# Performance work log

Hardware: AMD Instinct MI355X
Metric: run time of the kernel (lower is better)

The kernel has to match this reference:

```python
import jax, jax.numpy as jnp
import numpy as np
import math

SQRT2 = math.sqrt(2.0)
SQRT_2PI = math.sqrt(2.0 * math.pi)
T = 1.0


def _margin_from_bn(xt_flat):
    # xt_flat: [B, C*L]. torch .std() is unbiased (ddof=1).
    std = jnp.abs(jnp.std(xt_flat, axis=1, ddof=1))  # [B]
    mean = jnp.mean(xt_flat, axis=1)                  # [B]
    z = -mean / std
    cdf = 0.5 * (1.0 + jax.lax.erf(z / SQRT2))        # norm.cdf(-mean/std)
    safe_cdf = jnp.maximum(cdf, 1e-30)                # guard div; branch selected by where
    margin_a = -std * jnp.exp(-(mean / std) ** 2 / 2.0) / SQRT_2PI / safe_cdf + mean
    margin = jnp.where(cdf > 0.001, margin_a, -3.0 * std)
    # original detaches margin (computed on CPU via numpy/scipy)
    return jax.lax.stop_gradient(margin)


def reference(x_s, x_t, x_ts, x_st, i):
    B, C = x_ts.shape[0], x_ts.shape[1]
    xs = x_ts.reshape(B, C, -1)  # source: [B, C, L]
    xt = x_st.reshape(B, C, -1)  # target: [B, C, L]
    margin = _margin_from_bn(xt.reshape(B, -1))  # [B]
    # distillation_loss(source=xs, target=xt, T, dims=1, margin)
    target = jnp.maximum(xt / T, margin[:, None, None])
    entropy = jax.nn.softmax(xs / T, axis=1) * jax.nn.log_softmax(target / T, axis=1)
    channel_entropy = -jnp.sum(entropy, axis=1)          # [B, L]
    batch_mean_entropy = jnp.mean(channel_entropy, axis=1)  # [B]
    loss = jnp.mean(batch_mean_entropy)
    return (loss, entropy)


def setup_inputs() -> dict:
    key = jax.random.key(0)
    k1, k2, k3, k4 = jax.random.split(key, 4)
    return {
        "x_s": jax.random.normal(k1, (1,), dtype=jnp.float32),
        "x_t": jax.random.normal(k2, (1,), dtype=jnp.float32),
        "x_ts": jax.random.normal(k3, (8, 1024, 64, 64), dtype=jnp.float32),
        "x_st": jax.random.normal(k4, (8, 1024, 64, 64), dtype=jnp.float32),
        "i": 0,
    }
```

## Files before the change

kernel.cpp:

```cpp
#include <hip/hip_runtime.h>
#include <math.h>

#define BB 8
#define CC 1024
#define LL 4096
#define NPB (CC*LL)
#define LT 32


__global__ void k_batch_sums(const float* __restrict__ xt, double* __restrict__ sums) {
    int b = blockIdx.y;
    const float4* p = (const float4*)(xt + (size_t)b * NPB);
    int t = blockIdx.x * blockDim.x + threadIdx.x;
    double s1 = 0.0, s2 = 0.0;
    #pragma unroll
    for (int j4 = 0; j4 < 4; ++j4) {
        float4 v[4];
        #pragma unroll
        for (int k = 0; k < 4; ++k) v[k] = p[(size_t)(j4 * 4 + k) * 65536 + t];
        #pragma unroll
        for (int k = 0; k < 4; ++k) {
            float q1 = (v[k].x + v[k].y) + (v[k].z + v[k].w);
            float q2 = (v[k].x * v[k].x + v[k].y * v[k].y)
                     + (v[k].z * v[k].z + v[k].w * v[k].w);
            s1 += (double)q1;
            s2 += (double)q2;
        }
    }
    for (int off = 32; off; off >>= 1) {
        s1 += __shfl_down(s1, off, 64);
        s2 += __shfl_down(s2, off, 64);
    }
    __shared__ double ls1[4], ls2[4];
    int lane = threadIdx.x & 63, w = threadIdx.x >> 6;
    if (lane == 0) { ls1[w] = s1; ls2[w] = s2; }
    __syncthreads();
    if (threadIdx.x == 0) {
        atomicAdd(&sums[2 * b],     ls1[0] + ls1[1] + ls1[2] + ls1[3]);
        atomicAdd(&sums[2 * b + 1], ls2[0] + ls2[1] + ls2[2] + ls2[3]);
    }
}

__global__ __launch_bounds__(1024)
void k_fused(const float* __restrict__ xs, const float* __restrict__ xt,
             const double* __restrict__ sums,
             float* __restrict__ out1, double* __restrict__ lossAcc) {
    int tid = threadIdx.x;
    int b = blockIdx.y;
    int L0 = blockIdx.x * LT;
    int q = tid & 7;
    int g = tid >> 3;
    int lane = tid & 63, w = tid >> 6;

    __shared__ float s_mg;
    __shared__ __align__(16) float s_red[2][16][8][4];
    __shared__ __align__(16) float s_sinv[8][4];
    __shared__ __align__(16) float s_blog[8][4];
    __shared__ float wacc[16];

    if (tid == 0) {
        double n = (double)NPB;
        double s1 = sums[2 * b], s2 = sums[2 * b + 1];
        double mean = s1 / n;
        double var = (s2 - s1 * s1 / n) / (n - 1.0);
        double sd = sqrt(var);
        double z = -mean / sd;
        double cdf = 0.5 * (1.0 + erf(z / 1.4142135623730951));
        double safe = fmax(cdf, 1e-30);
        double r = mean / sd;
        double ma = -sd * exp(-r * r * 0.5) / 2.5066282746310002 / safe + mean;
        s_mg = (float)((cdf > 0.001) ? ma : -3.0 * sd);
    }
    __syncthreads();
    float mg = s_mg;

    const float* ps = xs + (size_t)b * NPB + L0 + q * 4;
    const float* pt = xt + (size_t)b * NPB + L0 + q * 4;

    float4 es[8], yv[8];
    float ss[4] = {0, 0, 0, 0}, sy[4] = {0, 0, 0, 0};
    #pragma unroll
    for (int i = 0; i < 8; ++i) {
        size_t off = (size_t)(g + 128 * i) * LL;
        float4 s4 = *(const float4*)(ps + off);
        float4 t4 = *(const float4*)(pt + off);
        float4 e, y;
        e.x = __expf(s4.x); e.y = __expf(s4.y); e.z = __expf(s4.z); e.w = __expf(s4.w);
        y.x = fmaxf(t4.x, mg); y.y = fmaxf(t4.y, mg);
        y.z = fmaxf(t4.z, mg); y.w = fmaxf(t4.w, mg);
        es[i] = e; yv[i] = y;
        ss[0] += e.x; ss[1] += e.y; ss[2] += e.z; ss[3] += e.w;
        sy[0] += __expf(y.x); sy[1] += __expf(y.y);
        sy[2] += __expf(y.z); sy[3] += __expf(y.w);
    }
    #pragma unroll
    for (int off = 8; off < 64; off <<= 1) {
        #pragma unroll
        for (int k = 0; k < 4; ++k) {
            ss[k] += __shfl_xor(ss[k], off, 64);
            sy[k] += __shfl_xor(sy[k], off, 64);
        }
    }
    if (lane < 8) {
        #pragma unroll
        for (int k = 0; k < 4; ++k) {
            s_red[0][w][lane][k] = ss[k];
            s_red[1][w][lane][k] = sy[k];
        }
    }
    __syncthreads();
    if (tid < 64) {
        int a  = tid >> 5;
        int qq = (tid >> 2) & 7;
        int k  = tid & 3;
        float t = 0.f;
        #pragma unroll
        for (int ww = 0; ww < 16; ++ww) t += s_red[a][ww][qq][k];
        if (a == 0) s_sinv[qq][k] = 1.0f / t;
        else        s_blog[qq][k] = __logf(t);
    }
    __syncthreads();
    float4 sinv = *(const float4*)&s_sinv[q][0];
    float4 blog = *(const float4*)&s_blog[q][0];

    float* po = out1 + (size_t)b * NPB + L0 + q * 4;
    float acc = 0.f;
    #pragma unroll
    for (int i = 0; i < 8; ++i) {
        size_t off = (size_t)(g + 128 * i) * LL;
        float4 e;
        e.x = es[i].x * sinv.x * (yv[i].x - blog.x);
        e.y = es[i].y * sinv.y * (yv[i].y - blog.y);
        e.z = es[i].z * sinv.z * (yv[i].z - blog.z);
        e.w = es[i].w * sinv.w * (yv[i].w - blog.w);
        *(float4*)(po + off) = e;
        acc += (e.x + e.y) + (e.z + e.w);
    }
    for (int off = 32; off; off >>= 1) acc += __shfl_down(acc, off, 64);
    if (lane == 0) wacc[w] = acc;
    __syncthreads();
    if (tid == 0) {
        double t = 0.0;
        #pragma unroll
        for (int ww = 0; ww < 16; ++ww) t += (double)wacc[ww];
        atomicAdd(lossAcc, t);
    }
}

__global__ void k_finalize(const double* __restrict__ lossAcc, float* __restrict__ out) {
    if (threadIdx.x == 0) out[0] = (float)(-lossAcc[0] / (double)(BB * LL));
}

extern "C" void kernel_launch(void* const* d_in, const int* in_sizes, int n_in,
                              void* d_out, int out_size, void* d_ws, size_t ws_size,
                              hipStream_t stream) {
    const float* x_ts = (const float*)d_in[2];
    const float* x_st = (const float*)d_in[3];
    float* out = (float*)d_out;

    double* sums    = (double*)d_ws;
    double* lossAcc = (double*)((char*)d_ws + 128);

    hipMemsetAsync(d_ws, 0, 256, stream);

    k_batch_sums<<<dim3(256, BB), 256, 0, stream>>>(x_st, sums);
    k_fused<<<dim3(LL / LT, BB), 1024, 0, stream>>>(x_ts, x_st, sums, out + 1, lossAcc);
    k_finalize<<<1, 64, 0, stream>>>(lossAcc, out);
}
```

Before: 391.6 us.

## Stage exp values in LDS, re-read target, halve tile and block size

The fused kernel now handles 16 columns per block with 512 threads, storing exp(source) in a 64KB shared buffer instead of registers. In the second pass it re-reads the target from global memory in reverse channel order, hoping for cache hits, and writes the output with nontemporal stores. The aim is to cut register pressure and raise occupancy. In exchange it adds global read traffic, and the large LDS footprint may limit how many blocks fit per CU.

```diff
diff --git a/kernel.cpp b/kernel.cpp
--- a/kernel.cpp
+++ b/kernel.cpp
@@ -5,7 +5,9 @@
 #define CC 1024
 #define LL 4096
 #define NPB (CC*LL)
-#define LT 32
+#define LT 16
+
+typedef float f32x4 __attribute__((ext_vector_type(4)));
 
 
 __global__ void k_batch_sums(const float* __restrict__ xt, double* __restrict__ sums) {
@@ -41,22 +43,23 @@
     }
 }
 
-__global__ __launch_bounds__(1024)
+__global__ __launch_bounds__(512, 4)
 void k_fused(const float* __restrict__ xs, const float* __restrict__ xt,
              const double* __restrict__ sums,
              float* __restrict__ out1, double* __restrict__ lossAcc) {
     int tid = threadIdx.x;
     int b = blockIdx.y;
     int L0 = blockIdx.x * LT;
-    int q = tid & 7;
-    int g = tid >> 3;
+    int q = tid & 3;
+    int g = tid >> 2;
     int lane = tid & 63, w = tid >> 6;
 
     __shared__ float s_mg;
-    __shared__ __align__(16) float s_red[2][16][8][4];
-    __shared__ __align__(16) float s_sinv[8][4];
-    __shared__ __align__(16) float s_blog[8][4];
-    __shared__ float wacc[16];
+    __shared__ __align__(16) float s_es[CC * LT];
+    __shared__ __align__(16) float s_red[2][8][4][4];
+    __shared__ __align__(16) float s_sinv[4][4];
+    __shared__ __align__(16) float s_blog[4][4];
+    __shared__ float wacc[8];
 
     if (tid == 0) {
         double n = (double)NPB;
@@ -77,31 +80,29 @@
     const float* ps = xs + (size_t)b * NPB + L0 + q * 4;
     const float* pt = xt + (size_t)b * NPB + L0 + q * 4;
 
-    float4 es[8], yv[8];
     float ss[4] = {0, 0, 0, 0}, sy[4] = {0, 0, 0, 0};
     #pragma unroll
     for (int i = 0; i < 8; ++i) {
-        size_t off = (size_t)(g + 128 * i) * LL;
+        int c = g + 128 * i;
+        size_t off = (size_t)c * LL;
         float4 s4 = *(const float4*)(ps + off);
         float4 t4 = *(const float4*)(pt + off);
-        float4 e, y;
+        float4 e;
         e.x = __expf(s4.x); e.y = __expf(s4.y); e.z = __expf(s4.z); e.w = __expf(s4.w);
-        y.x = fmaxf(t4.x, mg); y.y = fmaxf(t4.y, mg);
-        y.z = fmaxf(t4.z, mg); y.w = fmaxf(t4.w, mg);
-        es[i] = e; yv[i] = y;
+        *(float4*)&s_es[c * LT + q * 4] = e;
         ss[0] += e.x; ss[1] += e.y; ss[2] += e.z; ss[3] += e.w;
-        sy[0] += __expf(y.x); sy[1] += __expf(y.y);
-        sy[2] += __expf(y.z); sy[3] += __expf(y.w);
+        sy[0] += __expf(fmaxf(t4.x, mg)); sy[1] += __expf(fmaxf(t4.y, mg));
+        sy[2] += __expf(fmaxf(t4.z, mg)); sy[3] += __expf(fmaxf(t4.w, mg));
     }
     #pragma unroll
-    for (int off = 8; off < 64; off <<= 1) {
+    for (int off = 4; off < 64; off <<= 1) {
         #pragma unroll
         for (int k = 0; k < 4; ++k) {
             ss[k] += __shfl_xor(ss[k], off, 64);
             sy[k] += __shfl_xor(sy[k], off, 64);
         }
     }
-    if (lane < 8) {
+    if (lane < 4) {
         #pragma unroll
         for (int k = 0; k < 4; ++k) {
             s_red[0][w][lane][k] = ss[k];
@@ -109,13 +110,13 @@
         }
     }
     __syncthreads();
-    if (tid < 64) {
-        int a  = tid >> 5;
-        int qq = (tid >> 2) & 7;
+    if (tid < 32) {
+        int a  = tid >> 4;
+        int qq = (tid >> 2) & 3;
         int k  = tid & 3;
         float t = 0.f;
         #pragma unroll
-        for (int ww = 0; ww < 16; ++ww) t += s_red[a][ww][qq][k];
+        for (int ww = 0; ww < 8; ++ww) t += s_red[a][ww][qq][k];
         if (a == 0) s_sinv[qq][k] = 1.0f / t;
         else        s_blog[qq][k] = __logf(t);
     }
@@ -126,14 +127,17 @@
     float* po = out1 + (size_t)b * NPB + L0 + q * 4;
     float acc = 0.f;
     #pragma unroll
-    for (int i = 0; i < 8; ++i) {
-        size_t off = (size_t)(g + 128 * i) * LL;
-        float4 e;
-        e.x = es[i].x * sinv.x * (yv[i].x - blog.x);
-        e.y = es[i].y * sinv.y * (yv[i].y - blog.y);
-        e.z = es[i].z * sinv.z * (yv[i].z - blog.z);
-        e.w = es[i].w * sinv.w * (yv[i].w - blog.w);
-        *(float4*)(po + off) = e;
+    for (int i = 7; i >= 0; --i) {
+        int c = g + 128 * i;
+        size_t off = (size_t)c * LL;
+        float4 t4 = *(const float4*)(pt + off);
+        float4 ev = *(const float4*)&s_es[c * LT + q * 4];
+        f32x4 e;
+        e.x = ev.x * sinv.x * (fmaxf(t4.x, mg) - blog.x);
+        e.y = ev.y * sinv.y * (fmaxf(t4.y, mg) - blog.y);
+        e.z = ev.z * sinv.z * (fmaxf(t4.z, mg) - blog.z);
+        e.w = ev.w * sinv.w * (fmaxf(t4.w, mg) - blog.w);
+        __builtin_nontemporal_store(e, (f32x4*)(po + off));
         acc += (e.x + e.y) + (e.z + e.w);
     }
     for (int off = 32; off; off >>= 1) acc += __shfl_down(acc, off, 64);
@@ -142,7 +146,7 @@
     if (tid == 0) {
         double t = 0.0;
         #pragma unroll
-        for (int ww = 0; ww < 16; ++ww) t += (double)wacc[ww];
+        for (int ww = 0; ww < 8; ++ww) t += (double)wacc[ww];
         atomicAdd(lossAcc, t);
     }
 }
@@ -164,6 +168,6 @@
     hipMemsetAsync(d_ws, 0, 256, stream);
 
     k_batch_sums<<<dim3(256, BB), 256, 0, stream>>>(x_st, sums);
-    k_fused<<<dim3(LL / LT, BB), 1024, 0, stream>>>(x_ts, x_st, sums, out + 1, lossAcc);
+    k_fused<<<dim3(LL / LT, BB), 512, 0, stream>>>(x_ts, x_st, sums, out + 1, lossAcc);
     k_finalize<<<1, 64, 0, stream>>>(lossAcc, out);
 }
```

Measured after the change: 461.4 us. +17.8%, slower.
